# Optimization experiments

Measured on AMD Instinct MI355X. Metric: run time of the kernel, lower is better.

Reference implementation:

```python
import jax, jax.numpy as jnp
import numpy as np
from jax import lax

KS = 3  # kernel_size


def setup_inputs() -> dict:
    key = jax.random.key(0)
    k1, k2, k3 = jax.random.split(key, 3)
    B, D, C_IN, F = 4, 96, 16, 16
    feat = jax.random.normal(k1, (B, D, D, D, C_IN), dtype=jnp.float32)
    index = jax.random.randint(k2, (B, D, D, D), 0, 2, dtype=jnp.int32)
    # glorot-style scale for w [c_in * ks^3, filters]
    fan_in = C_IN * KS ** 3
    w = jax.random.normal(k3, (fan_in, F), dtype=jnp.float32) * jnp.float32(np.sqrt(2.0 / (fan_in + F)))
    b = jnp.zeros((F,), dtype=jnp.float32)
    return {"feat": feat, "index": index, "w": w, "b": b}


def reference(feat, index, w, b):
    # SparseConv: for every voxel where index != 0, gather the ks^3 neighborhood
    # (out-of-bounds neighbors read as zero), flatten to [N, ks^3 * C_in],
    # matmul with w, add b, and scatter back (zeros elsewhere).
    # The meshgrid('ij') offset order followed by reshape([-1, ks^3 * C_in])
    # makes w row index = ((dx*ks + dy)*ks + dz)*C_in + c_in, i.e. exactly a
    # dense 3-D cross-correlation kernel w.reshape(ks, ks, ks, C_in, F) with
    # SAME zero padding; the scatter_nd equals masking the output by index != 0.
    c_in = feat.shape[-1]
    filters = w.shape[-1]
    w_conv = w.reshape(KS, KS, KS, c_in, filters)  # DHWIO
    out = lax.conv_general_dilated(
        feat, w_conv,
        window_strides=(1, 1, 1),
        padding="SAME",
        dimension_numbers=("NDHWC", "DHWIO", "NDHWC"),
    ) + b
    mask = (index != 0)[..., None]  # [B, X, Y, Z, 1]
    return jnp.where(mask, out, jnp.zeros((), dtype=out.dtype))
```

## Files before the change

### kernel.cpp

```cpp
#include <hip/hip_runtime.h>

#define DSZ 96
#define CIN 16
#define NF  16
#define NXT (DSZ / 8)
#define NYT (DSZ / 4)
#define NZT (DSZ / 16)

typedef __attribute__((ext_vector_type(8))) short short8;
typedef __attribute__((ext_vector_type(4))) float f32x4;

union I4S8 { int4 i; short8 s; };

__global__ void pack_w(const float* __restrict__ w, short* __restrict__ wpack) {
  const int t = threadIdx.x >> 6;
  const int l = threadIdx.x & 63;
  const int tap = 2 * t + (l >> 5);
  const int cib = ((l >> 4) & 1) * 8;
  const int f = l & 15;
  short v[8];
#pragma unroll
  for (int j = 0; j < 8; ++j) {
    float x = (tap <= 26) ? w[(tap * 16 + cib + j) * 16 + f] : 0.0f;
    unsigned u = __float_as_uint(x);
    u = (u + 0x7FFFu + ((u >> 16) & 1u)) >> 16;
    v[j] = (short)u;
  }
  short8 s;
#pragma unroll
  for (int j = 0; j < 8; ++j) s[j] = v[j];
  reinterpret_cast<short8*>(wpack)[t * 64 + l] = s;
}

__global__ __launch_bounds__(512, 4) void conv_mfma_lds(
    const float* __restrict__ feat, const int* __restrict__ index,
    const float* __restrict__ bias, const short8* __restrict__ wpack,
    float* __restrict__ out) {
  __shared__ short smem[60 * 18 * 16];

  const int tid = threadIdx.x;
  const int lane = tid & 63;
  const int wid = tid >> 6;

  const int d = blockIdx.x;
  int L = (d & 7) * 864 + (d >> 3);
  const int yt = L % NYT;  L /= NYT;
  const int zt = L % NZT;  L /= NZT;
  const int xt = L % NXT;
  const int b  = L / NXT;
  const int x0 = xt * 8, y0 = yt * 4, z0 = zt * 16;

  short8 bw[14];
#pragma unroll
  for (int t = 0; t < 14; ++t) bw[t] = wpack[t * 64 + lane];

  for (int it = tid; it < 1080; it += 512) {
    const int col = it / 18;
    const int zp  = it - col * 18;
    const int colx = col / 6;
    const int coly = col - colx * 6;
    const int gx = x0 + colx - 1, gy = y0 + coly - 1, gz = z0 + zp - 1;
    const bool ok = ((unsigned)gx < (unsigned)DSZ) &
                    ((unsigned)gy < (unsigned)DSZ) &
                    ((unsigned)gz < (unsigned)DSZ);
    const long off = ok ? ((long)(((b * DSZ + gx) * DSZ + gy) * DSZ + gz) * CIN) : 0;
    const float4* p = reinterpret_cast<const float4*>(feat + off);
    float4 q0 = p[0], q1 = p[1], q2 = p[2], q3 = p[3];
    unsigned m0 = __builtin_amdgcn_perm(__float_as_uint(q0.y), __float_as_uint(q0.x), 0x07060302u);
    unsigned m1 = __builtin_amdgcn_perm(__float_as_uint(q0.w), __float_as_uint(q0.z), 0x07060302u);
    unsigned m2 = __builtin_amdgcn_perm(__float_as_uint(q1.y), __float_as_uint(q1.x), 0x07060302u);
    unsigned m3 = __builtin_amdgcn_perm(__float_as_uint(q1.w), __float_as_uint(q1.z), 0x07060302u);
    unsigned m4 = __builtin_amdgcn_perm(__float_as_uint(q2.y), __float_as_uint(q2.x), 0x07060302u);
    unsigned m5 = __builtin_amdgcn_perm(__float_as_uint(q2.w), __float_as_uint(q2.z), 0x07060302u);
    unsigned m6 = __builtin_amdgcn_perm(__float_as_uint(q3.y), __float_as_uint(q3.x), 0x07060302u);
    unsigned m7 = __builtin_amdgcn_perm(__float_as_uint(q3.w), __float_as_uint(q3.z), 0x07060302u);
    if (!ok) { m0 = m1 = m2 = m3 = m4 = m5 = m6 = m7 = 0u; }
    const int byte0 = (col * 576 + zp * 32) ^ ((zp & 4) << 2);
    *reinterpret_cast<int4*>((char*)smem + byte0)        = make_int4(m0, m1, m2, m3);
    *reinterpret_cast<int4*>((char*)smem + (byte0 ^ 16)) = make_int4(m4, m5, m6, m7);
  }

  const int cx = wid;
  const int tp = lane >> 5;
  int pre[3];
#pragma unroll
  for (int dz = 0; dz < 3; ++dz) {
    const int zp = (lane & 15) + dz;
    pre[dz] = (zp * 32 + (lane & 16)) ^ ((zp & 4) << 2);
  }
  int laddr[14];
#pragma unroll
  for (int t = 0; t < 14; ++t) {
    const int tapA = 2 * t;
    const int tapB = (2 * t + 1 <= 26) ? (2 * t + 1) : 26;
    const int aA = ((cx + tapA / 9) * 6 + (tapA / 3) % 3) * 576 + pre[tapA % 3];
    const int aB = ((cx + tapB / 9) * 6 + (tapB / 3) % 3) * 576 + pre[tapB % 3];
    laddr[t] = tp ? aB : aA;
  }

  const int fq = lane & 15, hq = lane >> 4;
  const float bf = bias[fq];
  const char* smb = (const char*)smem;

  const int vbase0 = ((b * DSZ + (x0 + cx)) * DSZ + y0) * DSZ + z0;
  const int* ip = index + vbase0 + hq * 4;
  float* op = out + (long)(vbase0 + hq * 4) * NF + fq;

  __syncthreads();

#pragma unroll 2
  for (int cy = 0; cy < 4; ++cy) {
    f32x4 acc0 = {0.f, 0.f, 0.f, 0.f};
    f32x4 acc1 = {0.f, 0.f, 0.f, 0.f};
#pragma unroll
    for (int t = 0; t < 14; ++t) {
      I4S8 u;
      u.i = *reinterpret_cast<const int4*>(smb + laddr[t] + cy * 576);
      if (t & 1)
        acc1 = __builtin_amdgcn_mfma_f32_16x16x32_bf16(u.s, bw[t], acc1, 0, 0, 0);
      else
        acc0 = __builtin_amdgcn_mfma_f32_16x16x32_bf16(u.s, bw[t], acc0, 0, 0, 0);
    }
    const int4 iv = *reinterpret_cast<const int4*>(ip);
    op[0 * NF] = iv.x ? (acc0[0] + acc1[0] + bf) : 0.0f;
    op[1 * NF] = iv.y ? (acc0[1] + acc1[1] + bf) : 0.0f;
    op[2 * NF] = iv.z ? (acc0[2] + acc1[2] + bf) : 0.0f;
    op[3 * NF] = iv.w ? (acc0[3] + acc1[3] + bf) : 0.0f;
    ip += DSZ;
    op += (long)DSZ * NF;
  }
}

__global__ __launch_bounds__(256) void sparse_conv_f32(
    const float* __restrict__ feat, const int* __restrict__ index,
    const float* __restrict__ w, const float* __restrict__ bias,
    float* __restrict__ out) {
  const int v = blockIdx.x * 256 + threadIdx.x;
  const int z = v % DSZ;
  int t = v / DSZ;
  const int y = t % DSZ; t /= DSZ;
  const int x = t % DSZ;
  const int bb = t / DSZ;
  float acc[NF];
#pragma unroll
  for (int f = 0; f < NF; ++f) acc[f] = bias[f];
  const bool active = (index[v] != 0);
#pragma unroll 1
  for (int kx = -1; kx <= 1; ++kx) {
    const int xx = x + kx;
    const bool okx = ((unsigned)xx < (unsigned)DSZ);
#pragma unroll 1
    for (int ky = -1; ky <= 1; ++ky) {
      const int yy = y + ky;
      const bool oky = okx && ((unsigned)yy < (unsigned)DSZ);
#pragma unroll 1
      for (int kz = -1; kz <= 1; ++kz) {
        const int zz = z + kz;
        const bool ok = oky && ((unsigned)zz < (unsigned)DSZ);
        const long long off = ((((long long)bb * DSZ + xx) * DSZ + yy) * DSZ + zz) * CIN;
        float4 q0, q1, q2, q3;
        if (ok) {
          const float4* fp = reinterpret_cast<const float4*>(feat + off);
          q0 = fp[0]; q1 = fp[1]; q2 = fp[2]; q3 = fp[3];
        } else {
          q0 = q1 = q2 = q3 = make_float4(0.f, 0.f, 0.f, 0.f);
        }
        const float fv[CIN] = {q0.x, q0.y, q0.z, q0.w, q1.x, q1.y, q1.z, q1.w,
                               q2.x, q2.y, q2.z, q2.w, q3.x, q3.y, q3.z, q3.w};
        const float* wr = w + ((((kx + 1) * 3 + (ky + 1)) * 3 + (kz + 1)) * CIN) * NF;
#pragma unroll
        for (int ci = 0; ci < CIN; ++ci) {
          const float fvv = fv[ci];
#pragma unroll
          for (int f = 0; f < NF; ++f) acc[f] = fmaf(fvv, wr[ci * NF + f], acc[f]);
        }
      }
    }
  }
  float4* op = reinterpret_cast<float4*>(out + (long long)v * NF);
  if (active) {
    op[0] = make_float4(acc[0], acc[1], acc[2], acc[3]);
    op[1] = make_float4(acc[4], acc[5], acc[6], acc[7]);
    op[2] = make_float4(acc[8], acc[9], acc[10], acc[11]);
    op[3] = make_float4(acc[12], acc[13], acc[14], acc[15]);
  } else {
    const float4 z4 = make_float4(0.f, 0.f, 0.f, 0.f);
    op[0] = z4; op[1] = z4; op[2] = z4; op[3] = z4;
  }
}

extern "C" void kernel_launch(void* const* d_in, const int* in_sizes, int n_in,
                              void* d_out, int out_size, void* d_ws, size_t ws_size,
                              hipStream_t stream) {
  const float* feat  = (const float*)d_in[0];
  const int*   index = (const int*)d_in[1];
  const float* w     = (const float*)d_in[2];
  const float* bias  = (const float*)d_in[3];
  float*       out   = (float*)d_out;

  const int nvox = in_sizes[1];

  if (ws_size < 14 * 64 * 8 * sizeof(short)) {
    sparse_conv_f32<<<nvox / 256, 256, 0, stream>>>(feat, index, w, bias, out);
    return;
  }

  short* wpack = (short*)d_ws;
  pack_w<<<1, 14 * 64, 0, stream>>>(w, wpack);

  const int blocks = 4 * NXT * NYT * NZT;
  conv_mfma_lds<<<blocks, 512, 0, stream>>>(feat, index, bias,
                                            (const short8*)wpack, out);
}
```

Measured before the change: 149.4 us.

## Make blocks persistent along z with double-buffered LDS staging

Each block now owns an 8x3 column tile in x,y and walks all six z tiles, staging the next 16-deep z slab into a second LDS buffer while computing the current one. The y tile shrinks from 4 to 3, so the halo is 5 columns instead of 6, and the weight registers and address setup are amortized over six slabs. This is meant to hide global-load latency and cut redundant halo loads and per-block setup. The cost is doubled LDS use, occupancy lowered to 2 blocks per CU, and a much smaller grid (1536 blocks), which may limit parallelism.

```diff
diff --git a/kernel.cpp b/kernel.cpp
--- a/kernel.cpp
+++ b/kernel.cpp
@@ -3,9 +3,7 @@
 #define DSZ 96
 #define CIN 16
 #define NF  16
-#define NXT (DSZ / 8)
-#define NYT (DSZ / 4)
-#define NZT (DSZ / 16)
+#define BUFB 28800
 
 typedef __attribute__((ext_vector_type(8))) short short8;
 typedef __attribute__((ext_vector_type(4))) float f32x4;
@@ -32,53 +30,57 @@
   reinterpret_cast<short8*>(wpack)[t * 64 + l] = s;
 }
 
-__global__ __launch_bounds__(512, 4) void conv_mfma_lds(
+__global__ __launch_bounds__(512, 2) void conv_mfma_zp(
     const float* __restrict__ feat, const int* __restrict__ index,
     const float* __restrict__ bias, const short8* __restrict__ wpack,
     float* __restrict__ out) {
-  __shared__ short smem[60 * 18 * 16];
+  __shared__ short smem[2 * 50 * 288];
 
   const int tid = threadIdx.x;
   const int lane = tid & 63;
   const int wid = tid >> 6;
 
   const int d = blockIdx.x;
-  int L = (d & 7) * 864 + (d >> 3);
-  const int yt = L % NYT;  L /= NYT;
-  const int zt = L % NZT;  L /= NZT;
-  const int xt = L % NXT;
-  const int b  = L / NXT;
-  const int x0 = xt * 8, y0 = yt * 4, z0 = zt * 16;
+  int L = (d & 7) * 192 + (d >> 3);
+  const int yt = L % 32;  L /= 32;
+  const int xt = L % 12;
+  const int b  = L / 12;
+  const int x0 = xt * 8, y0 = yt * 3;
 
   short8 bw[14];
 #pragma unroll
   for (int t = 0; t < 14; ++t) bw[t] = wpack[t * 64 + lane];
 
-  for (int it = tid; it < 1080; it += 512) {
-    const int col = it / 18;
-    const int zp  = it - col * 18;
-    const int colx = col / 6;
-    const int coly = col - colx * 6;
-    const int gx = x0 + colx - 1, gy = y0 + coly - 1, gz = z0 + zp - 1;
-    const bool ok = ((unsigned)gx < (unsigned)DSZ) &
-                    ((unsigned)gy < (unsigned)DSZ) &
-                    ((unsigned)gz < (unsigned)DSZ);
-    const long off = ok ? ((long)(((b * DSZ + gx) * DSZ + gy) * DSZ + gz) * CIN) : 0;
-    const float4* p = reinterpret_cast<const float4*>(feat + off);
-    float4 q0 = p[0], q1 = p[1], q2 = p[2], q3 = p[3];
-    unsigned m0 = __builtin_amdgcn_perm(__float_as_uint(q0.y), __float_as_uint(q0.x), 0x07060302u);
-    unsigned m1 = __builtin_amdgcn_perm(__float_as_uint(q0.w), __float_as_uint(q0.z), 0x07060302u);
-    unsigned m2 = __builtin_amdgcn_perm(__float_as_uint(q1.y), __float_as_uint(q1.x), 0x07060302u);
-    unsigned m3 = __builtin_amdgcn_perm(__float_as_uint(q1.w), __float_as_uint(q1.z), 0x07060302u);
-    unsigned m4 = __builtin_amdgcn_perm(__float_as_uint(q2.y), __float_as_uint(q2.x), 0x07060302u);
-    unsigned m5 = __builtin_amdgcn_perm(__float_as_uint(q2.w), __float_as_uint(q2.z), 0x07060302u);
-    unsigned m6 = __builtin_amdgcn_perm(__float_as_uint(q3.y), __float_as_uint(q3.x), 0x07060302u);
-    unsigned m7 = __builtin_amdgcn_perm(__float_as_uint(q3.w), __float_as_uint(q3.z), 0x07060302u);
-    if (!ok) { m0 = m1 = m2 = m3 = m4 = m5 = m6 = m7 = 0u; }
-    const int byte0 = (col * 576 + zp * 32) ^ ((zp & 4) << 2);
-    *reinterpret_cast<int4*>((char*)smem + byte0)        = make_int4(m0, m1, m2, m3);
-    *reinterpret_cast<int4*>((char*)smem + (byte0 ^ 16)) = make_int4(m4, m5, m6, m7);
-  }
+  auto stage = [&](int z0, int bufoff) {
+#pragma unroll
+    for (int k = 0; k < 2; ++k) {
+      const int i = tid + k * 512;
+      if (i < 900) {
+        const int col = i / 18;
+        const int zp  = i - col * 18;
+        const int colx = col / 5, coly = col - colx * 5;
+        const int gx = x0 + colx - 1, gy = y0 + coly - 1, gz = z0 + zp - 1;
+        const bool ok = ((unsigned)gx < (unsigned)DSZ) &
+                        ((unsigned)gy < (unsigned)DSZ) &
+                        ((unsigned)gz < (unsigned)DSZ);
+        const long off = ok ? ((long)(((b * DSZ + gx) * DSZ + gy) * DSZ + gz) * CIN) : 0;
+        const float4* p = reinterpret_cast<const float4*>(feat + off);
+        float4 q0 = p[0], q1 = p[1], q2 = p[2], q3 = p[3];
+        unsigned m0 = __builtin_amdgcn_perm(__float_as_uint(q0.y), __float_as_uint(q0.x), 0x07060302u);
+        unsigned m1 = __builtin_amdgcn_perm(__float_as_uint(q0.w), __float_as_uint(q0.z), 0x07060302u);
+        unsigned m2 = __builtin_amdgcn_perm(__float_as_uint(q1.y), __float_as_uint(q1.x), 0x07060302u);
+        unsigned m3 = __builtin_amdgcn_perm(__float_as_uint(q1.w), __float_as_uint(q1.z), 0x07060302u);
+        unsigned m4 = __builtin_amdgcn_perm(__float_as_uint(q2.y), __float_as_uint(q2.x), 0x07060302u);
+        unsigned m5 = __builtin_amdgcn_perm(__float_as_uint(q2.w), __float_as_uint(q2.z), 0x07060302u);
+        unsigned m6 = __builtin_amdgcn_perm(__float_as_uint(q3.y), __float_as_uint(q3.x), 0x07060302u);
+        unsigned m7 = __builtin_amdgcn_perm(__float_as_uint(q3.w), __float_as_uint(q3.z), 0x07060302u);
+        if (!ok) { m0 = m1 = m2 = m3 = m4 = m5 = m6 = m7 = 0u; }
+        const int byte0 = bufoff + ((col * 576 + zp * 32) ^ ((zp & 4) << 2));
+        *reinterpret_cast<int4*>((char*)smem + byte0)        = make_int4(m0, m1, m2, m3);
+        *reinterpret_cast<int4*>((char*)smem + (byte0 ^ 16)) = make_int4(m4, m5, m6, m7);
+      }
+    }
+  };
 
   const int cx = wid;
   const int tp = lane >> 5;
@@ -93,41 +95,47 @@
   for (int t = 0; t < 14; ++t) {
     const int tapA = 2 * t;
     const int tapB = (2 * t + 1 <= 26) ? (2 * t + 1) : 26;
-    const int aA = ((cx + tapA / 9) * 6 + (tapA / 3) % 3) * 576 + pre[tapA % 3];
-    const int aB = ((cx + tapB / 9) * 6 + (tapB / 3) % 3) * 576 + pre[tapB % 3];
+    const int aA = ((cx + tapA / 9) * 5 + (tapA / 3) % 3) * 576 + pre[tapA % 3];
+    const int aB = ((cx + tapB / 9) * 5 + (tapB / 3) % 3) * 576 + pre[tapB % 3];
     laddr[t] = tp ? aB : aA;
   }
 
   const int fq = lane & 15, hq = lane >> 4;
   const float bf = bias[fq];
   const char* smb = (const char*)smem;
-
-  const int vbase0 = ((b * DSZ + (x0 + cx)) * DSZ + y0) * DSZ + z0;
-  const int* ip = index + vbase0 + hq * 4;
-  float* op = out + (long)(vbase0 + hq * 4) * NF + fq;
-
+  const int rowbase = (b * DSZ + (x0 + cx)) * DSZ + y0;
+
+  auto compute = [&](int z0, int bufoff) {
+#pragma unroll
+    for (int cy = 0; cy < 3; ++cy) {
+      f32x4 acc0 = {0.f, 0.f, 0.f, 0.f};
+      f32x4 acc1 = {0.f, 0.f, 0.f, 0.f};
+#pragma unroll
+      for (int t = 0; t < 14; ++t) {
+        I4S8 u;
+        u.i = *reinterpret_cast<const int4*>(smb + bufoff + laddr[t] + cy * 576);
+        if (t & 1)
+          acc1 = __builtin_amdgcn_mfma_f32_16x16x32_bf16(u.s, bw[t], acc1, 0, 0, 0);
+        else
+          acc0 = __builtin_amdgcn_mfma_f32_16x16x32_bf16(u.s, bw[t], acc0, 0, 0, 0);
+      }
+      const int vb = (rowbase + cy) * DSZ + z0 + hq * 4;
+      const int4 iv = *reinterpret_cast<const int4*>(index + vb);
+      float* op = out + (long)vb * NF + fq;
+      op[0 * NF] = iv.x ? (acc0[0] + acc1[0] + bf) : 0.0f;
+      op[1 * NF] = iv.y ? (acc0[1] + acc1[1] + bf) : 0.0f;
+      op[2 * NF] = iv.z ? (acc0[2] + acc1[2] + bf) : 0.0f;
+      op[3 * NF] = iv.w ? (acc0[3] + acc1[3] + bf) : 0.0f;
+    }
+  };
+
+  stage(0, 0);
   __syncthreads();
-
-#pragma unroll 2
-  for (int cy = 0; cy < 4; ++cy) {
-    f32x4 acc0 = {0.f, 0.f, 0.f, 0.f};
-    f32x4 acc1 = {0.f, 0.f, 0.f, 0.f};
-#pragma unroll
-    for (int t = 0; t < 14; ++t) {
-      I4S8 u;
-      u.i = *reinterpret_cast<const int4*>(smb + laddr[t] + cy * 576);
-      if (t & 1)
-        acc1 = __builtin_amdgcn_mfma_f32_16x16x32_bf16(u.s, bw[t], acc1, 0, 0, 0);
-      else
-        acc0 = __builtin_amdgcn_mfma_f32_16x16x32_bf16(u.s, bw[t], acc0, 0, 0, 0);
-    }
-    const int4 iv = *reinterpret_cast<const int4*>(ip);
-    op[0 * NF] = iv.x ? (acc0[0] + acc1[0] + bf) : 0.0f;
-    op[1 * NF] = iv.y ? (acc0[1] + acc1[1] + bf) : 0.0f;
-    op[2 * NF] = iv.z ? (acc0[2] + acc1[2] + bf) : 0.0f;
-    op[3 * NF] = iv.w ? (acc0[3] + acc1[3] + bf) : 0.0f;
-    ip += DSZ;
-    op += (long)DSZ * NF;
+#pragma unroll
+  for (int zt = 0; zt < 6; ++zt) {
+    if (zt < 5) stage((zt + 1) * 16, ((zt + 1) & 1) * BUFB);
+    compute(zt * 16, (zt & 1) * BUFB);
+    __syncthreads();
   }
 }
 
@@ -208,7 +216,7 @@
   short* wpack = (short*)d_ws;
   pack_w<<<1, 14 * 64, 0, stream>>>(w, wpack);
 
-  const int blocks = 4 * NXT * NYT * NZT;
-  conv_mfma_lds<<<blocks, 512, 0, stream>>>(feat, index, bias,
-                                            (const short8*)wpack, out);
-}
+  const int blocks = 4 * 12 * 32;
+  conv_mfma_zp<<<blocks, 512, 0, stream>>>(feat, index, bias,
+                                           (const short8*)wpack, out);
+}
```

Result: faster. 144.0 us (-3.6%).
